# Kernel tuning notes

Measured on AMD Instinct MI355X. Metric: run time of the kernel, lower is better.

The kernel has to match this reference:

```python
import jax, jax.numpy as jnp
import numpy as np


def setup_inputs() -> dict:
    key = jax.random.key(0)
    k1, k2 = jax.random.split(key)
    B, V, D, C, F = 4, 50000, 16, 16, 16
    inputs = jax.random.normal(k1, (B, V, D, C), dtype=jnp.float32)
    # kernel shape (ndirs, nchannels, nfilters) as in build(); glorot-ish scale
    kernel = jax.random.normal(k2, (D, C, F), dtype=jnp.float32) * (1.0 / np.sqrt(D * C))
    bias = jnp.zeros((F,), dtype=jnp.float32)
    return {"inputs": inputs, "kernel": kernel, "bias": bias}


def reference(inputs, kernel, bias):
    # inputs: [B, V, D, C]; kernel: [D, C, F]; bias: [F]
    B, V, D, C = inputs.shape
    y = inputs.reshape(B * V, D, C)
    # circular extension along the direction axis: length 2*D-1
    y = jnp.concatenate([y, y[:, :-1, :]], axis=1)
    # valid conv1d with full-width kernel -> D outputs per vertex (circular correlation)
    y = jax.lax.conv_general_dilated(
        y, kernel, window_strides=(1,), padding="VALID",
        dimension_numbers=("NWC", "WIO", "NWC"))  # [B*V, D, F]
    y = y.reshape(B, V, D, -1) + bias  # bias add
    y = jax.nn.relu(y)
    # take_max=True: max-pool over the directions axis
    return jnp.max(y, axis=2)  # [B, V, F]
```

## Files before the change

### kernel.cpp

```cpp
#include <hip/hip_runtime.h>


typedef __attribute__((ext_vector_type(8))) short          bf16x8;
typedef __attribute__((ext_vector_type(4))) float          f32x4;
typedef __attribute__((ext_vector_type(8))) unsigned short us8;

__device__ __forceinline__ unsigned short f32_to_bf16(float f) {
    unsigned int u = __builtin_bit_cast(unsigned int, f);
    u += 0x7FFFu + ((u >> 16) & 1u);
    return (unsigned short)(u >> 16);
}

__device__ __forceinline__ bf16x8 cvt8(float4 a, float4 b) {
    bf16x8 r;
    r[0] = (short)f32_to_bf16(a.x); r[1] = (short)f32_to_bf16(a.y);
    r[2] = (short)f32_to_bf16(a.z); r[3] = (short)f32_to_bf16(a.w);
    r[4] = (short)f32_to_bf16(b.x); r[5] = (short)f32_to_bf16(b.y);
    r[6] = (short)f32_to_bf16(b.z); r[7] = (short)f32_to_bf16(b.w);
    return r;
}

__global__ __launch_bounds__(256) void build_wt(
    const float* __restrict__ kern,
    unsigned short* __restrict__ wh)
{
    int n = blockIdx.x;
    int k = threadIdx.x;
    int f = n >> 4, i = n & 15;
    int d = k >> 4, c = k & 15;
    int w = (d - i) & 15;
    wh[(n << 8) + k] = f32_to_bf16(kern[(w << 8) + (c << 4) + f]);
}


#define LOADX(buf, kc) {                                                      \
    _Pragma("unroll")                                                         \
    for (int h = 0; h < 2; ++h) {                                             \
        buf[0+h] = *(const float4*)(xrow0 + (kc)*64 +  0 + l4*8 + h*4);       \
        buf[2+h] = *(const float4*)(xrow0 + (kc)*64 + 32 + l4*8 + h*4);       \
        buf[4+h] = *(const float4*)(xrow1 + (kc)*64 +  0 + l4*8 + h*4);       \
        buf[6+h] = *(const float4*)(xrow1 + (kc)*64 + 32 + l4*8 + h*4);       \
    } }

#define COMPUTE(buf, kc) {                                                    \
    bf16x8 ah00 = cvt8(buf[0], buf[1]);                          \
    bf16x8 ah01 = cvt8(buf[2], buf[3]);                          \
    bf16x8 ah10 = cvt8(buf[4], buf[5]);                          \
    bf16x8 ah11 = cvt8(buf[6], buf[7]);                          \
    _Pragma("unroll")                                                         \
    for (int ks = 0; ks < 2; ++ks) {                                          \
        _Pragma("unroll")                                                     \
        for (int cn = 0; cn < 8; ++cn) {                                      \
            int n   = wn*128 + cn*16 + l15;                                   \
            int k   = (kc)*64 + ks*32 + l4*8;                                 \
            int idx = n*256 + (k ^ ((n & 7) << 3));                           \
            bf16x8 bh = *(const bf16x8*)(WH + idx);                           \
            acc[0][cn] = __builtin_amdgcn_mfma_f32_16x16x32_bf16(             \
                ks ? ah01 : ah00, bh, acc[0][cn], 0, 0, 0);                   \
            acc[1][cn] = __builtin_amdgcn_mfma_f32_16x16x32_bf16(             \
                ks ? ah11 : ah10, bh, acc[1][cn], 0, 0, 0);                   \
        }                                                                     \
    } }

__global__ __launch_bounds__(512) void ffconv_mfma(
    const float* __restrict__ x,
    const unsigned short* __restrict__ wh_g,
    const float* __restrict__ bias,
    float* __restrict__ out,
    int M)
{
    __shared__ unsigned short WH[256 * 256];
    __shared__ float OUTS[128 * 16];

    const int tid  = threadIdx.x;
    const int lane = tid & 63;
    const int wid  = tid >> 6;
    const int wm   = wid >> 1;
    const int wn   = wid & 1;
    const int l15  = lane & 15;
    const int l4   = lane >> 4;
    const int v0   = blockIdx.x * 128;

    int r0 = v0 + wm * 32 + l15;
    int r1 = r0 + 16;
    const float* xrow0 = x + (size_t)(r0 < M ? r0 : M - 1) * 256;
    const float* xrow1 = x + (size_t)(r1 < M ? r1 : M - 1) * 256;

    f32x4 acc[2][8];
    #pragma unroll
    for (int rm = 0; rm < 2; ++rm)
        #pragma unroll
        for (int cn = 0; cn < 8; ++cn)
            acc[rm][cn] = (f32x4){0.f, 0.f, 0.f, 0.f};

    float4 xa[8], xb[8];
    LOADX(xa, 0);

    #pragma unroll
    for (int p = 0; p < 16; ++p) {
        int e  = (p * 512 + tid) * 8;
        int n  = e >> 8;
        int k0 = e & 255;
        us8 v  = *(const us8*)(wh_g + n * 256 + k0);
        int idx = n * 256 + (k0 ^ ((n & 7) << 3));
        *(us8*)(WH + idx) = v;
    }
    __syncthreads();

    LOADX(xb, 1);
    COMPUTE(xa, 0);
    LOADX(xa, 2);
    COMPUTE(xb, 1);
    LOADX(xb, 3);
    COMPUTE(xa, 2);
    COMPUTE(xb, 3);

    #pragma unroll
    for (int rm = 0; rm < 2; ++rm) {
        #pragma unroll
        for (int cn = 0; cn < 8; ++cn) {
            float mx[4];
            #pragma unroll
            for (int q = 0; q < 4; ++q) {
                float v = acc[rm][cn][q];
                v = fmaxf(v, __shfl_xor(v, 1));
                v = fmaxf(v, __shfl_xor(v, 2));
                v = fmaxf(v, __shfl_xor(v, 4));
                v = fmaxf(v, __shfl_xor(v, 8));
                mx[q] = v;
            }
            if (l15 == 0) {
                int f = wn * 8 + cn;
                float bf = bias[f];
                #pragma unroll
                for (int q = 0; q < 4; ++q) {
                    int r = wm * 32 + rm * 16 + l4 * 4 + q;
                    OUTS[r * 16 + f] = fmaxf(mx[q] + bf, 0.f);
                }
            }
        }
    }
    __syncthreads();

    {
        int e  = tid * 4;
        int r  = e >> 4;
        int f0 = e & 15;
        if (v0 + r < M)
            *reinterpret_cast<float4*>(out + (size_t)(v0 + r) * 16 + f0) =
                *reinterpret_cast<const float4*>(OUTS + e);
    }
}

extern "C" void kernel_launch(void* const* d_in, const int* in_sizes, int n_in,
                              void* d_out, int out_size, void* d_ws, size_t ws_size,
                              hipStream_t stream) {
    const float* x    = (const float*)d_in[0];
    const float* kern = (const float*)d_in[1];
    const float* bias = (const float*)d_in[2];
    float* out        = (float*)d_out;

    unsigned short* wh = (unsigned short*)d_ws;

    const int M = in_sizes[0] / 256;

    hipLaunchKernelGGL(build_wt, dim3(256), dim3(256), 0, stream, kern, wh);

    const int blocks = (M + 127) / 128;
    hipLaunchKernelGGL(ffconv_mfma, dim3(blocks), dim3(512), 0, stream,
                       x, wh, bias, out, M);
}
```

Measured before the change: 352.5 us.

## Make MFMA conv kernel persistent with cross-tile prefetch via inline-asm loads

The grid becomes 256 persistent blocks that loop over 128-vertex tiles. The 128KB bf16 weight matrix is staged into LDS once per block instead of once per tile. Global loads are issued through inline asm with explicit vmcnt waits, so the next tile's input is prefetched while the current tile's last MFMAs and epilogue run. The costs are extra barriers per tile, heavier register pressure from double buffering, and fragile hand-placed waitcnt ordering.

```diff
diff --git a/kernel.cpp b/kernel.cpp
--- a/kernel.cpp
+++ b/kernel.cpp
@@ -11,12 +11,12 @@
     return (unsigned short)(u >> 16);
 }
 
-__device__ __forceinline__ bf16x8 cvt8(float4 a, float4 b) {
+__device__ __forceinline__ bf16x8 cvt8(f32x4 a, f32x4 b) {
     bf16x8 r;
-    r[0] = (short)f32_to_bf16(a.x); r[1] = (short)f32_to_bf16(a.y);
-    r[2] = (short)f32_to_bf16(a.z); r[3] = (short)f32_to_bf16(a.w);
-    r[4] = (short)f32_to_bf16(b.x); r[5] = (short)f32_to_bf16(b.y);
-    r[6] = (short)f32_to_bf16(b.z); r[7] = (short)f32_to_bf16(b.w);
+    r[0] = (short)f32_to_bf16(a[0]); r[1] = (short)f32_to_bf16(a[1]);
+    r[2] = (short)f32_to_bf16(a[2]); r[3] = (short)f32_to_bf16(a[3]);
+    r[4] = (short)f32_to_bf16(b[0]); r[5] = (short)f32_to_bf16(b[1]);
+    r[6] = (short)f32_to_bf16(b[2]); r[7] = (short)f32_to_bf16(b[3]);
     return r;
 }
 
@@ -32,42 +32,56 @@
     wh[(n << 8) + k] = f32_to_bf16(kern[(w << 8) + (c << 4) + f]);
 }
 
+#define GLD(dst, addr) \
+    asm volatile("global_load_dwordx4 %0, %1, off" : "=v"(dst) : "v"(addr))
 
-#define LOADX(buf, kc) {                                                      \
-    _Pragma("unroll")                                                         \
-    for (int h = 0; h < 2; ++h) {                                             \
-        buf[0+h] = *(const float4*)(xrow0 + (kc)*64 +  0 + l4*8 + h*4);       \
-        buf[2+h] = *(const float4*)(xrow0 + (kc)*64 + 32 + l4*8 + h*4);       \
-        buf[4+h] = *(const float4*)(xrow1 + (kc)*64 +  0 + l4*8 + h*4);       \
-        buf[6+h] = *(const float4*)(xrow1 + (kc)*64 + 32 + l4*8 + h*4);       \
-    } }
+#define VMWAIT(N) do { \
+    asm volatile("s_waitcnt vmcnt(" #N ")" ::: "memory"); \
+    __builtin_amdgcn_sched_barrier(0); } while (0)
 
-#define COMPUTE(buf, kc) {                                                    \
-    bf16x8 ah00 = cvt8(buf[0], buf[1]);                          \
-    bf16x8 ah01 = cvt8(buf[2], buf[3]);                          \
-    bf16x8 ah10 = cvt8(buf[4], buf[5]);                          \
-    bf16x8 ah11 = cvt8(buf[6], buf[7]);                          \
-    _Pragma("unroll")                                                         \
-    for (int ks = 0; ks < 2; ++ks) {                                          \
-        _Pragma("unroll")                                                     \
-        for (int cn = 0; cn < 8; ++cn) {                                      \
-            int n   = wn*128 + cn*16 + l15;                                   \
-            int k   = (kc)*64 + ks*32 + l4*8;                                 \
-            int idx = n*256 + (k ^ ((n & 7) << 3));                           \
-            bf16x8 bh = *(const bf16x8*)(WH + idx);                           \
-            acc[0][cn] = __builtin_amdgcn_mfma_f32_16x16x32_bf16(             \
-                ks ? ah01 : ah00, bh, acc[0][cn], 0, 0, 0);                   \
-            acc[1][cn] = __builtin_amdgcn_mfma_f32_16x16x32_bf16(             \
-                ks ? ah11 : ah10, bh, acc[1][cn], 0, 0, 0);                   \
-        }                                                                     \
-    } }
+#define ISSUE(buf, kc) { \
+    GLD(buf[0], xrow0 + (kc)*64 +  0 + l4*8); \
+    GLD(buf[1], xrow0 + (kc)*64 +  4 + l4*8); \
+    GLD(buf[2], xrow0 + (kc)*64 + 32 + l4*8); \
+    GLD(buf[3], xrow0 + (kc)*64 + 36 + l4*8); \
+    GLD(buf[4], xrow1 + (kc)*64 +  0 + l4*8); \
+    GLD(buf[5], xrow1 + (kc)*64 +  4 + l4*8); \
+    GLD(buf[6], xrow1 + (kc)*64 + 32 + l4*8); \
+    GLD(buf[7], xrow1 + (kc)*64 + 36 + l4*8); }
 
-__global__ __launch_bounds__(512) void ffconv_mfma(
+#define CVTS(buf) { \
+    ah00 = cvt8(buf[0], buf[1]);    \
+    ah01 = cvt8(buf[2], buf[3]);    \
+    ah10 = cvt8(buf[4], buf[5]);    \
+    ah11 = cvt8(buf[6], buf[7]); }
+
+#define MFMAS(kc) { \
+    _Pragma("unroll") \
+    for (int ks = 0; ks < 2; ++ks) { \
+        _Pragma("unroll") \
+        for (int cn = 0; cn < 8; ++cn) { \
+            int n   = wn*128 + cn*16 + l15; \
+            int k   = (kc)*64 + ks*32 + l4*8; \
+            int idx = n*256 + (k ^ ((n & 7) << 3)); \
+            bf16x8 bh = *(const bf16x8*)(WH + idx); \
+            acc[0][cn] = __builtin_amdgcn_mfma_f32_16x16x32_bf16( \
+                ks ? ah01 : ah00, bh, acc[0][cn], 0, 0, 0); \
+            acc[1][cn] = __builtin_amdgcn_mfma_f32_16x16x32_bf16( \
+                ks ? ah11 : ah10, bh, acc[1][cn], 0, 0, 0); \
+        } } }
+
+#define SETROWS(tt) { \
+    int rr0 = (tt)*128 + wm*32 + l15; \
+    int rr1 = rr0 + 16; \
+    xrow0 = x + (size_t)(rr0 < M ? rr0 : M - 1) * 256; \
+    xrow1 = x + (size_t)(rr1 < M ? rr1 : M - 1) * 256; }
+
+__global__ __launch_bounds__(512, 2) void ffconv_mfma(
     const float* __restrict__ x,
     const unsigned short* __restrict__ wh_g,
     const float* __restrict__ bias,
     float* __restrict__ out,
-    int M)
+    int M, int nt)
 {
     __shared__ unsigned short WH[256 * 256];
     __shared__ float OUTS[128 * 16];
@@ -79,22 +93,20 @@
     const int wn   = wid & 1;
     const int l15  = lane & 15;
     const int l4   = lane >> 4;
-    const int v0   = blockIdx.x * 128;
+    const int G    = gridDim.x;
 
-    int r0 = v0 + wm * 32 + l15;
-    int r1 = r0 + 16;
-    const float* xrow0 = x + (size_t)(r0 < M ? r0 : M - 1) * 256;
-    const float* xrow1 = x + (size_t)(r1 < M ? r1 : M - 1) * 256;
+    float bv[8];
+    #pragma unroll
+    for (int cn = 0; cn < 8; ++cn) bv[cn] = bias[wn * 8 + cn];
 
+    const float *xrow0, *xrow1;
+    f32x4 xa[8], xb[8];
     f32x4 acc[2][8];
-    #pragma unroll
-    for (int rm = 0; rm < 2; ++rm)
-        #pragma unroll
-        for (int cn = 0; cn < 8; ++cn)
-            acc[rm][cn] = (f32x4){0.f, 0.f, 0.f, 0.f};
+    bf16x8 ah00, ah01, ah10, ah11;
 
-    float4 xa[8], xb[8];
-    LOADX(xa, 0);
+    SETROWS(blockIdx.x);
+    ISSUE(xa, 0);
+    ISSUE(xb, 1);
 
     #pragma unroll
     for (int p = 0; p < 16; ++p) {
@@ -107,48 +119,59 @@
     }
     __syncthreads();
 
-    LOADX(xb, 1);
-    COMPUTE(xa, 0);
-    LOADX(xa, 2);
-    COMPUTE(xb, 1);
-    LOADX(xb, 3);
-    COMPUTE(xa, 2);
-    COMPUTE(xb, 3);
+    for (int t = blockIdx.x; t < nt; t += G) {
+        #pragma unroll
+        for (int rm = 0; rm < 2; ++rm)
+            #pragma unroll
+            for (int cn = 0; cn < 8; ++cn)
+                acc[rm][cn] = (f32x4){0.f, 0.f, 0.f, 0.f};
 
-    #pragma unroll
-    for (int rm = 0; rm < 2; ++rm) {
+        VMWAIT(8);  CVTS(xa);  ISSUE(xa, 2);  MFMAS(0);
+        VMWAIT(8);  CVTS(xb);  ISSUE(xb, 3);  MFMAS(1);
+        VMWAIT(8);  CVTS(xa);  MFMAS(2);
+        VMWAIT(0);  CVTS(xb);
+        {
+            int tn = t + G;
+            if (tn < nt) { SETROWS(tn); ISSUE(xa, 0); ISSUE(xb, 1); }
+        }
+        MFMAS(3);
+
         #pragma unroll
-        for (int cn = 0; cn < 8; ++cn) {
-            float mx[4];
+        for (int rm = 0; rm < 2; ++rm) {
             #pragma unroll
-            for (int q = 0; q < 4; ++q) {
-                float v = acc[rm][cn][q];
-                v = fmaxf(v, __shfl_xor(v, 1));
-                v = fmaxf(v, __shfl_xor(v, 2));
-                v = fmaxf(v, __shfl_xor(v, 4));
-                v = fmaxf(v, __shfl_xor(v, 8));
-                mx[q] = v;
-            }
-            if (l15 == 0) {
-                int f = wn * 8 + cn;
-                float bf = bias[f];
+            for (int cn = 0; cn < 8; ++cn) {
+                float mx[4];
                 #pragma unroll
                 for (int q = 0; q < 4; ++q) {
-                    int r = wm * 32 + rm * 16 + l4 * 4 + q;
-                    OUTS[r * 16 + f] = fmaxf(mx[q] + bf, 0.f);
+                    float v = acc[rm][cn][q];
+                    v = fmaxf(v, __shfl_xor(v, 1));
+                    v = fmaxf(v, __shfl_xor(v, 2));
+                    v = fmaxf(v, __shfl_xor(v, 4));
+                    v = fmaxf(v, __shfl_xor(v, 8));
+                    mx[q] = v;
+                }
+                if (l15 == 0) {
+                    int f = wn * 8 + cn;
+                    #pragma unroll
+                    for (int q = 0; q < 4; ++q) {
+                        int r = wm * 32 + rm * 16 + l4 * 4 + q;
+                        OUTS[r * 16 + f] = fmaxf(mx[q] + bv[cn], 0.f);
+                    }
                 }
             }
         }
-    }
-    __syncthreads();
+        __syncthreads();
 
-    {
-        int e  = tid * 4;
-        int r  = e >> 4;
-        int f0 = e & 15;
-        if (v0 + r < M)
-            *reinterpret_cast<float4*>(out + (size_t)(v0 + r) * 16 + f0) =
-                *reinterpret_cast<const float4*>(OUTS + e);
+        {
+            int e  = tid * 4;
+            int r  = e >> 4;
+            int f0 = e & 15;
+            int v0 = t * 128;
+            if (v0 + r < M)
+                *reinterpret_cast<float4*>(out + (size_t)(v0 + r) * 16 + f0) =
+                    *reinterpret_cast<const float4*>(OUTS + e);
+        }
+        __syncthreads();
     }
 }
 
@@ -162,11 +185,11 @@
 
     unsigned short* wh = (unsigned short*)d_ws;
 
-    const int M = in_sizes[0] / 256;
+    const int M  = in_sizes[0] / 256;
+    const int nt = (M + 127) / 128;
 
     hipLaunchKernelGGL(build_wt, dim3(256), dim3(256), 0, stream, kern, wh);
 
-    const int blocks = (M + 127) / 128;
-    hipLaunchKernelGGL(ffconv_mfma, dim3(blocks), dim3(512), 0, stream,
-                       x, wh, bias, out, M);
+    hipLaunchKernelGGL(ffconv_mfma, dim3(256), dim3(512), 0, stream,
+                       x, wh, bias, out, M, nt);
 }
```

After: 320.4 us. -9.1%, faster.
